# Kernel tuning notes

Hardware: AMD Instinct MI355X
Metric: run time of the kernel (lower is better)

## Reference

```python
import jax, jax.numpy as jnp
import numpy as np

B, P, F, E, H, V = 128, 196, 2048, 512, 1024, 10000
TMAX = 30  # max(captions_len) - 1 decode steps
BN_EPS = 1e-5


def setup_inputs() -> dict:
    key = jax.random.key(0)
    ks = jax.random.split(key, 14)
    encoder_feat = jax.random.normal(ks[0], (B, P, F), jnp.float32)
    gt_captions = jax.random.randint(ks[1], (B, TMAX + 1), 0, V, dtype=jnp.int32)
    lens = jax.random.randint(ks[2], (B,), 2, TMAX + 2, dtype=jnp.int32)
    lens = lens.at[0].set(TMAX + 1)
    captions_len = jnp.sort(lens)[::-1]  # sorted descending, as the torch slicing assumes
    embedding = jax.random.uniform(ks[3], (V, E), jnp.float32, -0.1, 0.1)
    W_init = jax.random.normal(ks[4], (E, F), jnp.float32) * np.sqrt(2.0 / F)
    b_init = jnp.zeros((E,), jnp.float32)
    bn_gamma = jnp.ones((E,), jnp.float32)
    bn_beta = jnp.zeros((E,), jnp.float32)
    s = 1.0 / np.sqrt(H)
    W_ih = jax.random.uniform(ks[5], (4 * H, E), jnp.float32, -s, s)
    b_ih = jax.random.uniform(ks[6], (4 * H,), jnp.float32, -s, s)
    W_hh = jax.random.uniform(ks[7], (4 * H, H), jnp.float32, -s, s)
    b_hh = jax.random.uniform(ks[8], (4 * H,), jnp.float32, -s, s)
    W_fc = jax.random.normal(ks[9], (V, H), jnp.float32) * np.sqrt(2.0 / H)
    b_fc = jnp.zeros((V,), jnp.float32)
    return {
        'encoder_feat': encoder_feat, 'gt_captions': gt_captions, 'captions_len': captions_len,
        'embedding': embedding, 'W_init': W_init, 'b_init': b_init,
        'bn_gamma': bn_gamma, 'bn_beta': bn_beta,
        'W_ih': W_ih, 'b_ih': b_ih, 'W_hh': W_hh, 'b_hh': b_hh,
        'W_fc': W_fc, 'b_fc': b_fc,
    }


def _lstm_cell(h, c, x, W_ih, b_ih, W_hh, b_hh):
    # PyTorch LSTMCell: gates = x W_ih^T + b_ih + h W_hh^T + b_hh, order [i, f, g, o]
    gates = x @ W_ih.T + b_ih + h @ W_hh.T + b_hh
    i, f, g, o = jnp.split(gates, 4, axis=-1)
    c_new = jax.nn.sigmoid(f) * c + jax.nn.sigmoid(i) * jnp.tanh(g)
    h_new = jax.nn.sigmoid(o) * jnp.tanh(c_new)
    return h_new, c_new


def reference(encoder_feat, gt_captions, captions_len, embedding, W_init, b_init,
              bn_gamma, bn_beta, W_ih, b_ih, W_hh, b_hh, W_fc, b_fc):
    batch = encoder_feat.shape[0]
    hidden = W_hh.shape[1]
    # t == 0: image feature -> sigmoid(linear) -> BatchNorm1d (eval: rm=0, rv=1)
    feat = encoder_feat.mean(axis=1)                      # [B, F]
    x0 = jax.nn.sigmoid(feat @ W_init.T + b_init)         # [B, E]
    x0 = bn_gamma * (x0 / jnp.sqrt(1.0 + BN_EPS)) + bn_beta
    h0 = jnp.zeros((batch, hidden), x0.dtype)
    c0 = jnp.zeros((batch, hidden), x0.dtype)
    h, c = _lstm_cell(h0, c0, x0, W_ih, b_ih, W_hh, b_hh)
    # decode steps t = 1..TMAX over ground-truth token embeddings
    emb = embedding[gt_captions[:, :TMAX]]                # [B, T, E]
    xs = jnp.swapaxes(emb, 0, 1)                          # [T, B, E]

    def step(carry, x_t):
        h, c = carry
        h, c = _lstm_cell(h, c, x_t, W_ih, b_ih, W_hh, b_hh)
        preds = h @ W_fc.T + b_fc                         # [B, V]
        return (h, c), preds

    _, preds = jax.lax.scan(step, (h, c), xs)             # [T, B, V]
    preds = jnp.swapaxes(preds, 0, 1)                     # [B, T, V]
    # rows beyond batch_size_t were never written in torch (zeros tensor) -> mask
    mask = jnp.arange(TMAX)[None, :] < (captions_len - 1)[:, None]  # [B, T]
    return jnp.where(mask[:, :, None], preds, 0.0)
```

## Files before the change

kernel.cpp:

```cpp
#include <hip/hip_runtime.h>
#include <math.h>

typedef __bf16 bf16;
typedef __bf16 bf16x8 __attribute__((ext_vector_type(8)));
typedef __bf16 bf16x4 __attribute__((ext_vector_type(4)));
typedef float f32x4 __attribute__((ext_vector_type(4)));

#define MFMA_B16(a,b,c) __builtin_amdgcn_mfma_f32_16x16x32_bf16((a),(b),(c),0,0,0)

constexpr int TMAXc = 30;
constexpr int Bc = 128, Pc = 196, Fc = 2048, Ec = 512, Hc = 1024, Vc = 10000;
constexpr int G4c = 4 * Hc;
constexpr int NSTEP = TMAXc + 1;
constexpr int MALLc = NSTEP * Bc;
constexpr int MOUTc = TMAXc * Bc;
constexpr int NBLK = 256;

__device__ __forceinline__ float fsigm(float x){
  return __fdividef(1.0f, 1.0f + __expf(-x));
}
__device__ __forceinline__ float ftanh(float x){
  return 1.0f - __fdividef(2.0f, __expf(2.0f*x) + 1.0f);
}

__device__ __forceinline__ void gll16(const void* g, void* l){
  __builtin_amdgcn_global_load_lds((const __attribute__((address_space(1))) void*)g,
                                   (__attribute__((address_space(3))) void*)l, 16, 0, 0);
}

__device__ __forceinline__ void wt16(bf16* p, bf16x8 v){
  asm volatile("global_store_dwordx4 %0, %1, off sc0 sc1" :: "v"(p), "v"(v) : "memory");
}

__device__ __forceinline__ int aldf(int* f){
  return __hip_atomic_load(f, __ATOMIC_RELAXED, __HIP_MEMORY_SCOPE_AGENT);
}

__device__ __forceinline__ void waitflag(int* f, int tgt){
  long long t0 = __builtin_amdgcn_s_memrealtime();
  while (aldf(f) < tgt) {
    __builtin_amdgcn_s_sleep(1);
    if (__builtin_amdgcn_s_memrealtime() - t0 > 100000) break;
  }
}

__device__ __forceinline__ void waitflags4(int* F, int& f1, int& f2, int& f3){
  long long t0 = __builtin_amdgcn_s_memrealtime();
  for (;;) {
    int f0 = aldf(F + 0);
    f1 = aldf(F + 1);
    f2 = aldf(F + 2);
    f3 = aldf(F + 3);
    if (f0 >= 32) break;
    __builtin_amdgcn_s_sleep(1);
    if (__builtin_amdgcn_s_memrealtime() - t0 > 100000) break;
  }
}


__global__ void mean_kernel(const float* __restrict__ enc, bf16* __restrict__ feat){
  int blk = blockIdx.x, b = blk >> 1, half = blk & 1;
  int f0 = half*1024 + threadIdx.x*4;
  const float* p = enc + (size_t)b*Pc*Fc + f0;
  float4 s = {0.f,0.f,0.f,0.f};
  #pragma unroll 4
  for (int q = 0; q < Pc; ++q) {
    float4 v = *(const float4*)(p + (size_t)q*Fc);
    s.x += v.x; s.y += v.y; s.z += v.z; s.w += v.w;
  }
  const float r = 1.0f/(float)Pc;
  bf16x4 o = { (bf16)(s.x*r), (bf16)(s.y*r), (bf16)(s.z*r), (bf16)(s.w*r) };
  *(bf16x4*)&feat[b*Fc + f0] = o;
}

__global__ void conv_kernel(const float* __restrict__ src, bf16* __restrict__ dst, int n4){
  int i = blockIdx.x*256 + threadIdx.x;
  if (i >= n4) return;
  float4 v = ((const float4*)src)[i];
  bf16x4 o = { (bf16)v.x, (bf16)v.y, (bf16)v.z, (bf16)v.w };
  *(bf16x4*)&dst[i*4] = o;
}

__global__ void permconv_ih(const float* __restrict__ W, bf16* __restrict__ Wp){
  int i = blockIdx.x*256 + threadIdx.x;
  if (i >= G4c*Ec/4) return;
  int i4 = i*4;
  int rp = i4 >> 9, k = i4 & 511;
  int g = rp & 3, j = rp >> 2;
  float4 v = *(const float4*)&W[(size_t)(g*Hc + j)*Ec + k];
  bf16x4 o = { (bf16)v.x, (bf16)v.y, (bf16)v.z, (bf16)v.w };
  *(bf16x4*)&Wp[i4] = o;
}

__global__ void permsplit_hh(const float* __restrict__ W, bf16* __restrict__ Whi, bf16* __restrict__ Wlo){
  int i = blockIdx.x*256 + threadIdx.x;
  if (i >= G4c*Hc/4) return;
  int i4 = i*4;
  int rp = i4 >> 10, k = i4 & 1023;
  int g = rp & 3, j = rp >> 2;
  float4 v = *(const float4*)&W[(size_t)(g*Hc + j)*Hc + k];
  bf16 h0=(bf16)v.x, h1=(bf16)v.y, h2=(bf16)v.z, h3=(bf16)v.w;
  bf16x4 hi = { h0, h1, h2, h3 };
  bf16x4 lo = { (bf16)(v.x-(float)h0), (bf16)(v.y-(float)h1), (bf16)(v.z-(float)h2), (bf16)(v.w-(float)h3) };
  *(bf16x4*)&Whi[i4] = hi;
  *(bf16x4*)&Wlo[i4] = lo;
}

__global__ void split_kernel(const float* __restrict__ W, bf16* __restrict__ Whi, bf16* __restrict__ Wlo, int n4){
  int i = blockIdx.x*256 + threadIdx.x;
  if (i >= n4) return;
  float4 v = ((const float4*)W)[i];
  bf16 h0=(bf16)v.x, h1=(bf16)v.y, h2=(bf16)v.z, h3=(bf16)v.w;
  bf16x4 hi = { h0, h1, h2, h3 };
  bf16x4 lo = { (bf16)(v.x-(float)h0), (bf16)(v.y-(float)h1), (bf16)(v.z-(float)h2), (bf16)(v.w-(float)h3) };
  *(bf16x4*)&Whi[i*4] = hi;
  *(bf16x4*)&Wlo[i*4] = lo;
}

__global__ void bcomb_kernel(const float* __restrict__ bih, const float* __restrict__ bhh, float* __restrict__ bc){
  int i = blockIdx.x*256 + threadIdx.x;
  if (i >= G4c) return;
  int g = i & 3, j = i >> 2;
  bc[i] = bih[g*Hc + j] + bhh[g*Hc + j];
}

__global__ void gather_kernel(const float* __restrict__ emb, const int* __restrict__ gt, bf16* __restrict__ X){
  int idx = blockIdx.x*256 + threadIdx.x;
  if (idx >= MOUTc*(Ec/4)) return;
  int r = idx >> 7, ei = (idx & 127) * 4;
  int s = (r >> 7) + 1, b = r & 127;
  int tok = gt[b*(TMAXc+1) + (s-1)];
  float4 v = *(const float4*)(emb + (size_t)tok*Ec + ei);
  bf16x4 o = { (bf16)v.x, (bf16)v.y, (bf16)v.z, (bf16)v.w };
  *(bf16x4*)&X[(size_t)(s*Bc + b)*Ec + ei] = o;
}

__global__ void build_ridx(const int* __restrict__ lens, int* __restrict__ meta){
  int i = blockIdx.x*256 + threadIdx.x;
  if (i >= MOUTc) return;
  int t = i >> 7, b = i & 127;
  int S = 0, R = 0;
  for (int bb = 0; bb < 128; ++bb) {
    int l = lens[bb] - 1;
    S += (t < l) ? t : l;
    R += l;
  }
  if (i == 0) meta[0] = R;
  if (i >= R) meta[1 + i] = 0;
  if (t < lens[b] - 1) meta[1 + S + b] = i;
}

__global__ void zerofill(const int* __restrict__ lens, float* __restrict__ out){
  int i = blockIdx.x*256 + threadIdx.x;
  if (i >= MOUTc*2500) return;
  int row = i / 2500, c4 = i - row*2500;
  int b = row / TMAXc, t = row - b*TMAXc;
  if (t >= lens[b] - 1) {
    float4 z = {0.f,0.f,0.f,0.f};
    *(float4*)(out + (size_t)row*Vc + c4*4) = z;
  }
}

__global__ __launch_bounds__(256, 2) void initA(
  const bf16* __restrict__ feat, const bf16* __restrict__ Wi, float* __restrict__ part)
{
  __shared__ alignas(16) bf16 sA[128*32], sB[128*32];
  int tid = threadIdx.x, lane = tid & 63, w = tid >> 6, wr = w >> 1, wc = w & 1;
  int nt = blockIdx.x & 3, kc = blockIdx.x >> 2;
  int n0 = nt*128;

  f32x4 acc[4][4] = {};
  for (int kt = kc*256; kt < kc*256 + 256; kt += 32) {
    #pragma unroll
    for (int is = 0; is < 2; ++is) {
      int p = tid*16 + is*4096;
      int r = p >> 6, c = (p & 63) >> 1;
      int ldsoff = w*512 + is*2048;
      gll16(feat + (size_t)r*Fc + kt + c, &sA[ldsoff]);
      gll16(Wi + (size_t)(n0 + r)*Fc + kt + c, &sB[ldsoff]);
    }
    __syncthreads();
    int koff = (lane >> 4) * 8;
    bf16x8 ah[4], bh[4];
    #pragma unroll
    for (int mi = 0; mi < 4; ++mi)
      ah[mi] = *(const bf16x8*)&sA[(wr*64 + mi*16 + (lane & 15))*32 + koff];
    #pragma unroll
    for (int ni = 0; ni < 4; ++ni)
      bh[ni] = *(const bf16x8*)&sB[(wc*64 + ni*16 + (lane & 15))*32 + koff];
    #pragma unroll
    for (int mi = 0; mi < 4; ++mi)
      #pragma unroll
      for (int ni = 0; ni < 4; ++ni)
        acc[mi][ni] = MFMA_B16(ah[mi], bh[ni], acc[mi][ni]);
    __syncthreads();
  }
  #pragma unroll
  for (int mi = 0; mi < 4; ++mi)
    #pragma unroll
    for (int ni = 0; ni < 4; ++ni) {
      int lrow = wr*64 + mi*16 + ((lane >> 4) << 2);
      int col = n0 + wc*64 + ni*16 + (lane & 15);
      #pragma unroll
      for (int j = 0; j < 4; ++j)
        part[((size_t)kc*128 + lrow + j)*512 + col] = acc[mi][ni][j];
    }
}

__global__ void initB(const float* __restrict__ part, const float* __restrict__ binit,
                      const float* __restrict__ gam, const float* __restrict__ bet,
                      bf16* __restrict__ Xall)
{
  int i = blockIdx.x*256 + threadIdx.x;
  if (i >= 128*512) return;
  int col = i & 511;
  float v = 0.f;
  #pragma unroll
  for (int kc = 0; kc < 8; ++kc) v += part[(size_t)kc*128*512 + i];
  const float rbn = rsqrtf(1.0f + 1e-5f);
  v = fsigm(v + binit[col]);
  v = gam[col]*(v*rbn) + bet[col];
  Xall[i] = (bf16)v;
}

template<int EPI, bool SPLIT, bool XSWZ>
__global__ __launch_bounds__(256, 2) void gemm_kernel(
  const bf16* __restrict__ Ahi, const bf16* __restrict__ Alo,
  const bf16* __restrict__ Bhi, const bf16* __restrict__ Blo,
  int M, int N, int K, int mtiles,
  const float* __restrict__ p0,
  bf16* __restrict__ outb, float* __restrict__ outf, const int* __restrict__ meta)
{
  constexpr int BK = 32;
  __shared__ alignas(16) bf16 sAh[128*BK], sBh[128*BK];
  __shared__ alignas(16) bf16 sAl[SPLIT ? 128*BK : 8], sBl[SPLIT ? 128*BK : 8];

  int tid = threadIdx.x;
  int lane = tid & 63, w = tid >> 6, wr = w >> 1, wc = w & 1;
  int bid = blockIdx.x;
  if constexpr (XSWZ) {
    int nwg = gridDim.x, q = nwg >> 3, r = nwg & 7;
    int x = bid & 7, o = bid >> 3;
    bid = (x < r ? x*(q+1) : r*(q+1) + (x-r)*q) + o;
  }
  int nt = bid / mtiles, mt = bid - nt*mtiles;
  int m0 = mt*128, n0 = nt*128;

  int R = M;
  if constexpr (EPI == 2) {
    R = meta[0];
    if (m0 >= R) return;
  }

  int sr = (tid*16) >> 6;
  int gr0, gr1;
  if constexpr (EPI == 2) { gr0 = meta[1 + m0 + sr]; gr1 = meta[1 + m0 + sr + 64]; }
  else                    { gr0 = m0 + sr;           gr1 = m0 + sr + 64; }

  f32x4 acc[4][4] = {};

  for (int kt = 0; kt < K; kt += BK) {
    #pragma unroll
    for (int is = 0; is < 2; ++is) {
      int p = tid*16 + is*4096;
      int r = p >> 6, c = (p & 63) >> 1;
      int ldsoff = w*512 + is*2048;
      int ga = is ? gr1 : gr0;
      gll16(Ahi + (size_t)ga*K + kt + c, &sAh[ldsoff]);
      int rb = n0 + r; rb = rb < N ? rb : N - 1;
      gll16(Bhi + (size_t)rb*K + kt + c, &sBh[ldsoff]);
      if constexpr (SPLIT) {
        gll16(Alo + (size_t)ga*K + kt + c, &sAl[ldsoff]);
        gll16(Blo + (size_t)rb*K + kt + c, &sBl[ldsoff]);
      }
    }
    __syncthreads();

    int koff = (lane >> 4) * 8;
    bf16x8 ah[4], bh[4], al[SPLIT?4:1], bl[SPLIT?4:1];
    #pragma unroll
    for (int mi = 0; mi < 4; ++mi) {
      int rr = wr*64 + mi*16 + (lane & 15);
      ah[mi] = *(const bf16x8*)&sAh[rr*BK + koff];
      if constexpr (SPLIT) al[mi] = *(const bf16x8*)&sAl[rr*BK + koff];
    }
    #pragma unroll
    for (int ni = 0; ni < 4; ++ni) {
      int rr = wc*64 + ni*16 + (lane & 15);
      bh[ni] = *(const bf16x8*)&sBh[rr*BK + koff];
      if constexpr (SPLIT) bl[ni] = *(const bf16x8*)&sBl[rr*BK + koff];
    }
    #pragma unroll
    for (int mi = 0; mi < 4; ++mi)
      #pragma unroll
      for (int ni = 0; ni < 4; ++ni) {
        acc[mi][ni] = MFMA_B16(ah[mi], bh[ni], acc[mi][ni]);
        if constexpr (SPLIT) {
          acc[mi][ni] = MFMA_B16(ah[mi], bl[ni], acc[mi][ni]);
          acc[mi][ni] = MFMA_B16(al[mi], bh[ni], acc[mi][ni]);
        }
      }
    __syncthreads();
  }

  #pragma unroll
  for (int mi = 0; mi < 4; ++mi) {
    #pragma unroll
    for (int ni = 0; ni < 4; ++ni) {
      int lrow = m0 + wr*64 + mi*16 + ((lane >> 4) << 2);
      int col = n0 + wc*64 + ni*16 + (lane & 15);
      #pragma unroll
      for (int j = 0; j < 4; ++j) {
        int rr = lrow + j;
        float v = acc[mi][ni][j];
        if constexpr (EPI == 1) {
          outb[(size_t)rr*G4c + col] = (bf16)(v + p0[col]);
        } else {
          if (rr < R && col < N) {
            int val = meta[1 + rr];
            int t = val >> 7, b = val & 127;
            outf[(size_t)b*(TMAXc*Vc) + (size_t)t*Vc + col] = v + p0[col];
          }
        }
      }
    }
  }
}


__global__ __launch_bounds__(256, 1) void lstm_persist(
  const bf16* __restrict__ Whi, const bf16* __restrict__ Wlo,
  const bf16* __restrict__ Xg,
  bf16* __restrict__ hCh, bf16* __restrict__ hCl,
  bf16* __restrict__ Hh, bf16* __restrict__ Hl,
  const int* __restrict__ lens,
  int* __restrict__ flg)
{
  extern __shared__ char sWc[];
  int tid = threadIdx.x, lane = tid & 63, w = tid >> 6;
  int bid = blockIdx.x;
  int strip = bid >> 1, rh = bid & 1;
  int pc0 = strip * 32;
  int row0 = rh * 64 + w * 16;
  int grp = strip >> 5;
  char* scr = sWc + 131072 + w*512;

  for (int ch = tid; ch < 4096; ch += 256) {
    int p = ch >> 7;
    int k = (ch & 127) * 8;
    bf16x8 vh = *(const bf16x8*)&Whi[(size_t)(pc0 + p)*Hc + k];
    bf16x8 vl = *(const bf16x8*)&Wlo[(size_t)(pc0 + p)*Hc + k];
    int be = (p*Hc + k)*2;
    int sw = (p & 7) << 4;
    *(bf16x8*)(sWc + (be ^ sw)) = vh;
    *(bf16x8*)(sWc + ((be + 65536) ^ sw)) = vl;
  }
  __syncthreads();

  int bp = lane & 15;
  int bk = (lane >> 4) << 3;
  int bswz = (bp & 7) << 4;
  int rbase = row0 + ((lane >> 4) << 2);
  int e = lane & 3;

  int Lh = lens[rh * 64];
  if (Lh > NSTEP) Lh = NSTEP;
  int lenv = lens[row0 + (lane & 15)] - 1;

  float creg[2][4] = {};
  float xgv[2][4];
  #pragma unroll
  for (int ni = 0; ni < 2; ++ni)
    #pragma unroll
    for (int j = 0; j < 4; ++j)
      xgv[ni][j] = (float)Xg[(size_t)(rbase + j)*G4c + pc0 + ni*16 + bp];

#define GATEQ(g, fg) do { if (s > 0) { \
    if (tid == 0 && (fg) < 32) waitflag(&flg[(s*2 + rh)*4 + (g)], 32); \
    __builtin_amdgcn_s_barrier(); \
    asm volatile("" ::: "memory"); } } while (0)

#define LOADQ(qh, ql, g) do { \
    _Pragma("unroll") \
    for (int i = 0; i < 8; ++i) { \
      qh[i] = *(const bf16x8*)(pah + ((g)*8 + i)*32); \
      ql[i] = *(const bf16x8*)(pal + ((g)*8 + i)*32); \
    } \
    asm volatile("" ::: "memory"); } while (0)

#define MFMAQ(qh, ql, g) do { \
    _Pragma("unroll") \
    for (int i = 0; i < 8; ++i) { \
      int ks = (g)*8 + i; \
      _Pragma("unroll") \
      for (int ni = 0; ni < 2; ++ni) { \
        int be = ((ni*16 + bp)*Hc + ks*32 + bk)*2; \
        bf16x8 bvh = *(const bf16x8*)(sWc + (be ^ bswz)); \
        bf16x8 bvl = *(const bf16x8*)(sWc + ((be + 65536) ^ bswz)); \
        aHH[ni] = MFMA_B16(qh[i], bvh, aHH[ni]); \
        aHL[ni] = MFMA_B16(qh[i], bvl, aHL[ni]); \
        aLH[ni] = MFMA_B16(ql[i], bvh, aLH[ni]); \
      } \
    } } while (0)

  #pragma unroll 1
  for (int s = 0; s < Lh; ++s) {
    const bf16* pah = hCh + (size_t)s*Bc*Hc + (size_t)(row0 + bp)*Hc + bk;
    const bf16* pal = hCl + (size_t)s*Bc*Hc + (size_t)(row0 + bp)*Hc + bk;
    bf16* hwh = hCh + (size_t)(s+1)*Bc*Hc;
    bf16* hwl = hCl + (size_t)(s+1)*Bc*Hc;

    f32x4 aHH[2], aHL[2], aLH[2];
    #pragma unroll
    for (int ni = 0; ni < 2; ++ni) {
      #pragma unroll
      for (int j = 0; j < 4; ++j) aHH[ni][j] = xgv[ni][j];
      aHL[ni] = (f32x4){0.f,0.f,0.f,0.f};
      aLH[ni] = (f32x4){0.f,0.f,0.f,0.f};
    }

    bf16x8 qh0[8], ql0[8], qh1[8], ql1[8];
    int f1 = 32, f2 = 32, f3 = 32;

    if (s > 0) {
      if (tid == 0) waitflags4(&flg[(s*2 + rh)*4], f1, f2, f3);
      __builtin_amdgcn_s_barrier();
      asm volatile("" ::: "memory");
    }
    LOADQ(qh0, ql0, 0);
    GATEQ(1, f1); LOADQ(qh1, ql1, 1);
    MFMAQ(qh0, ql0, 0);
    GATEQ(2, f2); LOADQ(qh0, ql0, 2);
    MFMAQ(qh1, ql1, 1);
    GATEQ(3, f3); LOADQ(qh1, ql1, 3);
    MFMAQ(qh0, ql0, 2);
    MFMAQ(qh1, ql1, 3);

    #pragma unroll
    for (int ni = 0; ni < 2; ++ni) {
      #pragma unroll
      for (int j = 0; j < 4; ++j) {
        float v = aHH[ni][j] + aHL[ni][j] + aLH[ni][j];
        float a  = v;
        float b1 = __shfl_xor(v, 1);
        float c2 = __shfl_xor(v, 2);
        float d3 = __shfl_xor(v, 3);
        int m;
        m = e;     float gI = (m==0)?a:(m==1)?b1:(m==2)?c2:d3;
        m = e ^ 1; float gF = (m==0)?a:(m==1)?b1:(m==2)?c2:d3;
        m = e ^ 2; float gG = (m==0)?a:(m==1)?b1:(m==2)?c2:d3;
        m = e ^ 3; float gO = (m==0)?a:(m==1)?b1:(m==2)?c2:d3;

        float co = creg[ni][j];
        float cn = fsigm(gF)*co + fsigm(gI)*ftanh(gG);
        float hn = fsigm(gO)*ftanh(cn);
        creg[ni][j] = cn;
        bf16 hhi = (bf16)hn;
        int r16 = ((lane >> 4) << 2) + j;
        int c8  = ni*4 + (bp >> 2);
        if (e == 1)      *(bf16*)(scr + (r16*8 + c8)*2) = hhi;
        else if (e == 2) *(bf16*)(scr + 256 + (r16*8 + c8)*2) = (bf16)(hn - (float)hhi);
      }
    }

    asm volatile("s_waitcnt lgkmcnt(0)" ::: "memory");
    __builtin_amdgcn_sched_barrier(0);

    if (lane < 32) {
      int r = lane & 15, buf = lane >> 4;
      bf16x8 vv = *(const bf16x8*)(scr + buf*256 + r*16);
      bf16* dst = (buf ? hwl : hwh) + (size_t)(row0 + r)*Hc + strip*8;
      wt16(dst, vv);
    }

    __syncthreads();
    if (tid == 0 && s + 1 < Lh)
      __hip_atomic_fetch_add(&flg[((s+1)*2 + rh)*4 + grp], 1,
                             __ATOMIC_RELAXED, __HIP_MEMORY_SCOPE_AGENT);

    if (s > 0 && lane >= 32 && (s - 1) < lenv) {
      int r = lane & 15, buf = (lane >> 4) & 1;
      bf16x8 vv = *(const bf16x8*)(scr + buf*256 + r*16);
      *(bf16x8*)((buf ? Hl : Hh) + (size_t)((s-1)*Bc + row0 + r)*Hc + strip*8) = vv;
    }
    if (s + 1 < Lh) {
      #pragma unroll
      for (int ni = 0; ni < 2; ++ni)
        #pragma unroll
        for (int j = 0; j < 4; ++j)
          xgv[ni][j] = (float)Xg[(size_t)((s+1)*Bc + rbase + j)*G4c + pc0 + ni*16 + bp];
    }
  }
#undef GATEQ
#undef LOADQ
#undef MFMAQ
}


extern "C" void kernel_launch(void* const* d_in, const int* in_sizes, int n_in,
                              void* d_out, int out_size, void* d_ws, size_t ws_size,
                              hipStream_t stream)
{
  const float* enc   = (const float*)d_in[0];
  const int*   gt    = (const int*)  d_in[1];
  const int*   lens  = (const int*)  d_in[2];
  const float* emb   = (const float*)d_in[3];
  const float* Winit = (const float*)d_in[4];
  const float* binit = (const float*)d_in[5];
  const float* gam   = (const float*)d_in[6];
  const float* bet   = (const float*)d_in[7];
  const float* Wih   = (const float*)d_in[8];
  const float* bih   = (const float*)d_in[9];
  const float* Whh   = (const float*)d_in[10];
  const float* bhh   = (const float*)d_in[11];
  const float* Wfc   = (const float*)d_in[12];
  const float* bfc   = (const float*)d_in[13];
  float* out = (float*)d_out;

  char* ws = (char*)d_ws;
  size_t off = 0;
  auto alloc = [&](size_t bytes) -> char* {
    char* p = ws + off;
    off += (bytes + 255) & ~(size_t)255;
    return p;
  };

  bf16* featB  = (bf16*)alloc((size_t)Bc*Fc*2);
  bf16* WinitB = (bf16*)alloc((size_t)Ec*Fc*2);
  bf16* WihpB  = (bf16*)alloc((size_t)G4c*Ec*2);
  bf16* WhhHi  = (bf16*)alloc((size_t)G4c*Hc*2);
  bf16* WhhLo  = (bf16*)alloc((size_t)G4c*Hc*2);
  bf16* WfcHi  = (bf16*)alloc((size_t)Vc*Hc*2);
  bf16* WfcLo  = (bf16*)alloc((size_t)Vc*Hc*2);
  float* bcomb = (float*)alloc((size_t)G4c*4);
  bf16* Xall   = (bf16*)alloc((size_t)MALLc*Ec*2);
  bf16* Xg     = (bf16*)alloc((size_t)MALLc*G4c*2);
  bf16* hChH   = (bf16*)alloc((size_t)(NSTEP+1)*Bc*Hc*2);
  bf16* hChL   = (bf16*)alloc((size_t)(NSTEP+1)*Bc*Hc*2);
  bf16* HallH  = (bf16*)alloc((size_t)MOUTc*Hc*2);
  bf16* HallL  = (bf16*)alloc((size_t)MOUTc*Hc*2);
  float* part  = (float*)alloc((size_t)8*128*512*4);
  int*  meta   = (int*) alloc((size_t)(1 + MOUTc)*4);
  int*  flg    = (int*) alloc((size_t)256*4);

  if (off > ws_size) return;

  hipMemsetAsync(hChH, 0, (size_t)Bc*Hc*2, stream);
  hipMemsetAsync(hChL, 0, (size_t)Bc*Hc*2, stream);
  hipMemsetAsync(flg, 0, (size_t)256*4, stream);

  mean_kernel<<<256, 256, 0, stream>>>(enc, featB);
  conv_kernel<<<(Ec*Fc/4 + 255)/256, 256, 0, stream>>>(Winit, WinitB, Ec*Fc/4);
  permconv_ih<<<(G4c*Ec/4 + 255)/256, 256, 0, stream>>>(Wih, WihpB);
  permsplit_hh<<<(G4c*Hc/4 + 255)/256, 256, 0, stream>>>(Whh, WhhHi, WhhLo);
  split_kernel<<<(Vc*Hc/4 + 255)/256, 256, 0, stream>>>(Wfc, WfcHi, WfcLo, Vc*Hc/4);
  bcomb_kernel<<<(G4c + 255)/256, 256, 0, stream>>>(bih, bhh, bcomb);
  gather_kernel<<<(MOUTc*(Ec/4) + 255)/256, 256, 0, stream>>>(emb, gt, Xall);
  build_ridx<<<(MOUTc + 255)/256, 256, 0, stream>>>(lens, meta);
  zerofill<<<(MOUTc*2500 + 255)/256, 256, 0, stream>>>(lens, out);

  initA<<<32, 256, 0, stream>>>(featB, WinitB, part);
  initB<<<(128*512 + 255)/256, 256, 0, stream>>>(part, binit, gam, bet, Xall);

  gemm_kernel<1,false,true><<<31*32, 256, 0, stream>>>(
      Xall, nullptr, WihpB, nullptr, MALLc, G4c, Ec, 31,
      bcomb, Xg, nullptr, nullptr);

  hipFuncSetAttribute(reinterpret_cast<const void*>(lstm_persist),
                      hipFuncAttributeMaxDynamicSharedMemorySize, 133120);
  lstm_persist<<<NBLK, 256, 133120, stream>>>(
      WhhHi, WhhLo, Xg, hChH, hChL, HallH, HallL, lens, flg);

  gemm_kernel<2,true,true><<<79*30, 256, 0, stream>>>(
      HallH, HallL, WfcHi, WfcLo, MOUTc, Vc, Hc, 30,
      bfc, nullptr, out, meta);
}
```

Baseline: 739.8 us.

## Pre-tile recurrent weights in LDS and transpose gate cells across lanes

The W_hh strip is now stored in LDS in MFMA-fragment order, so each lane reads contiguous 16-byte chunks at a fixed lane offset instead of computing XOR-swizzled addresses per access. The gate epilogue uses a 4x4 lane transpose via shuffles, so each lane computes one LSTM cell per column group instead of all four lanes redundantly computing four cells each. This cuts transcendental work and shuffles in the per-step epilogue and simplifies LDS addressing. The cell-state register layout changes to one value per lane per column group, which must match the new transpose mapping.

```diff
diff --git a/kernel.cpp b/kernel.cpp
--- a/kernel.cpp
+++ b/kernel.cpp
@@ -21,6 +21,11 @@
 }
 __device__ __forceinline__ float ftanh(float x){
   return 1.0f - __fdividef(2.0f, __expf(2.0f*x) + 1.0f);
+}
+__device__ __forceinline__ float sel4(float a, float b, float c, float d, int i){
+  float x = (i & 1) ? b : a;
+  float y = (i & 1) ? d : c;
+  return (i & 2) ? y : x;
 }
 
 __device__ __forceinline__ void gll16(const void* g, void* l){
@@ -348,26 +353,28 @@
   for (int ch = tid; ch < 4096; ch += 256) {
     int p = ch >> 7;
     int k = (ch & 127) * 8;
+    int ni = p >> 4, bp = p & 15;
+    int ks = k >> 5, kg = (k >> 3) & 3;
+    int off = (((ks*2 + ni)*4 + kg)*16 + bp) * 16;
     bf16x8 vh = *(const bf16x8*)&Whi[(size_t)(pc0 + p)*Hc + k];
     bf16x8 vl = *(const bf16x8*)&Wlo[(size_t)(pc0 + p)*Hc + k];
-    int be = (p*Hc + k)*2;
-    int sw = (p & 7) << 4;
-    *(bf16x8*)(sWc + (be ^ sw)) = vh;
-    *(bf16x8*)(sWc + ((be + 65536) ^ sw)) = vl;
+    *(bf16x8*)(sWc + off) = vh;
+    *(bf16x8*)(sWc + 65536 + off) = vl;
   }
   __syncthreads();
 
   int bp = lane & 15;
   int bk = (lane >> 4) << 3;
-  int bswz = (bp & 7) << 4;
   int rbase = row0 + ((lane >> 4) << 2);
   int e = lane & 3;
+  const char* sWhiB = sWc + lane*16;
+  const char* sWloB = sWc + 65536 + lane*16;
 
   int Lh = lens[rh * 64];
   if (Lh > NSTEP) Lh = NSTEP;
   int lenv = lens[row0 + (lane & 15)] - 1;
 
-  float creg[2][4] = {};
+  float creg[2] = {0.f, 0.f};
   float xgv[2][4];
   #pragma unroll
   for (int ni = 0; ni < 2; ++ni)
@@ -394,9 +401,8 @@
       int ks = (g)*8 + i; \
       _Pragma("unroll") \
       for (int ni = 0; ni < 2; ++ni) { \
-        int be = ((ni*16 + bp)*Hc + ks*32 + bk)*2; \
-        bf16x8 bvh = *(const bf16x8*)(sWc + (be ^ bswz)); \
-        bf16x8 bvl = *(const bf16x8*)(sWc + ((be + 65536) ^ bswz)); \
+        bf16x8 bvh = *(const bf16x8*)(sWhiB + (ks*2 + ni)*1024); \
+        bf16x8 bvl = *(const bf16x8*)(sWloB + (ks*2 + ni)*1024); \
         aHH[ni] = MFMA_B16(qh[i], bvh, aHH[ni]); \
         aHL[ni] = MFMA_B16(qh[i], bvl, aHL[ni]); \
         aLH[ni] = MFMA_B16(ql[i], bvh, aLH[ni]); \
@@ -438,29 +444,28 @@
 
     #pragma unroll
     for (int ni = 0; ni < 2; ++ni) {
-      #pragma unroll
-      for (int j = 0; j < 4; ++j) {
-        float v = aHH[ni][j] + aHL[ni][j] + aLH[ni][j];
-        float a  = v;
-        float b1 = __shfl_xor(v, 1);
-        float c2 = __shfl_xor(v, 2);
-        float d3 = __shfl_xor(v, 3);
-        int m;
-        m = e;     float gI = (m==0)?a:(m==1)?b1:(m==2)?c2:d3;
-        m = e ^ 1; float gF = (m==0)?a:(m==1)?b1:(m==2)?c2:d3;
-        m = e ^ 2; float gG = (m==0)?a:(m==1)?b1:(m==2)?c2:d3;
-        m = e ^ 3; float gO = (m==0)?a:(m==1)?b1:(m==2)?c2:d3;
-
-        float co = creg[ni][j];
-        float cn = fsigm(gF)*co + fsigm(gI)*ftanh(gG);
-        float hn = fsigm(gO)*ftanh(cn);
-        creg[ni][j] = cn;
-        bf16 hhi = (bf16)hn;
-        int r16 = ((lane >> 4) << 2) + j;
-        int c8  = ni*4 + (bp >> 2);
-        if (e == 1)      *(bf16*)(scr + (r16*8 + c8)*2) = hhi;
-        else if (e == 2) *(bf16*)(scr + 256 + (r16*8 + c8)*2) = (bf16)(hn - (float)hhi);
-      }
+      float v0 = aHH[ni][0] + aHL[ni][0] + aLH[ni][0];
+      float v1 = aHH[ni][1] + aHL[ni][1] + aLH[ni][1];
+      float v2 = aHH[ni][2] + aHL[ni][2] + aLH[ni][2];
+      float v3 = aHH[ni][3] + aHL[ni][3] + aLH[ni][3];
+      float g0 = sel4(v0, v1, v2, v3, e);
+      float g1 = __shfl_xor(sel4(v0, v1, v2, v3, e ^ 1), 1);
+      float g2 = __shfl_xor(sel4(v0, v1, v2, v3, e ^ 2), 2);
+      float g3 = __shfl_xor(sel4(v0, v1, v2, v3, e ^ 3), 3);
+      float gI = sel4(g0, g1, g2, g3, e);
+      float gF = sel4(g0, g1, g2, g3, e ^ 1);
+      float gG = sel4(g0, g1, g2, g3, e ^ 2);
+      float gO = sel4(g0, g1, g2, g3, e ^ 3);
+
+      float co = creg[ni];
+      float cn = fsigm(gF)*co + fsigm(gI)*ftanh(gG);
+      float hn = fsigm(gO)*ftanh(cn);
+      creg[ni] = cn;
+      bf16 hhi = (bf16)hn;
+      int r16 = ((lane >> 4) << 2) + e;
+      int c8  = ni*4 + (bp >> 2);
+      *(bf16*)(scr + (r16*8 + c8)*2) = hhi;
+      *(bf16*)(scr + 256 + (r16*8 + c8)*2) = (bf16)(hn - (float)hhi);
     }
 
     asm volatile("s_waitcnt lgkmcnt(0)" ::: "memory");
```

After: 646.0 us. -12.7%, faster.
